# Optimization experiments

Hardware: AMD Instinct MI355X
Metric: run time of the kernel (lower is better)

## Reference

```python
import jax, jax.numpy as jnp
import numpy as np

N_NODES = 50000
N_EDGES = 800000
N_GRAPHS = 64
IN_DIM = 128
HID = 128
S, C = 4, 16
DIM1 = 3 * S * S  # 48
OUT_DIM = DIM1 * C  # 768


def gcn_conv(x, W, b, src, dst, w):
    """PyG GCNConv: linear transform, then sym-normalized aggregation with self-loops (weight 1)."""
    n = x.shape[0]
    h = x @ W  # [N, out]
    deg = jnp.zeros((n,), x.dtype).at[dst].add(w) + 1.0  # self-loop weight 1
    dinv = jax.lax.rsqrt(deg)
    norm = dinv[src] * w * dinv[dst]  # [E]
    agg = jnp.zeros_like(h).at[dst].add(h[src] * norm[:, None])
    agg = agg + h * (1.0 / deg)[:, None]  # self-loop messages
    return agg + b


def setup_inputs() -> dict:
    key = jax.random.key(0)
    ks = jax.random.split(key, 16)
    x = jax.random.normal(ks[0], (N_NODES, IN_DIM), jnp.float32)
    edge_index = jax.random.randint(ks[1], (2, N_EDGES), 0, N_NODES, jnp.int64)
    edge_attr = jax.random.uniform(ks[2], (N_EDGES,), jnp.float32)
    batch = jnp.sort(jax.random.randint(ks[3], (N_NODES,), 0, N_GRAPHS, jnp.int64))

    def glorot(k, fan_in, fan_out):
        s = np.sqrt(6.0 / (fan_in + fan_out)).astype(np.float32)
        return jax.random.uniform(k, (fan_in, fan_out), jnp.float32, -s, s)

    return {
        "x": x, "edge_index": edge_index, "edge_attr": edge_attr, "batch": batch,
        "W1": glorot(ks[4], IN_DIM, HID), "b1": jnp.zeros((HID,), jnp.float32),
        "W2": glorot(ks[5], HID, HID // 2), "b2": jnp.zeros((HID // 2,), jnp.float32),
        "W3": glorot(ks[6], HID // 2, HID // 4), "b3": jnp.zeros((HID // 4,), jnp.float32),
        "Wl": glorot(ks[7], HID // 4, OUT_DIM), "bl": jnp.zeros((OUT_DIM,), jnp.float32),
    }


def reference(x, edge_index, edge_attr, batch, W1, b1, W2, b2, W3, b3, Wl, bl):
    src, dst = edge_index[0], edge_index[1]
    w = edge_attr / edge_attr.max()
    h = jax.nn.relu(gcn_conv(x, W1, b1, src, dst, w))
    h = jax.nn.relu(gcn_conv(h, W2, b2, src, dst, w))
    h = jax.nn.relu(gcn_conv(h, W3, b3, src, dst, w))
    # global mean pool over graphs
    sums = jax.ops.segment_sum(h, batch, num_segments=N_GRAPHS)
    cnt = jax.ops.segment_sum(jnp.ones((h.shape[0],), h.dtype), batch, num_segments=N_GRAPHS)
    pooled = sums / jnp.maximum(cnt, 1.0)[:, None]
    out = pooled @ Wl + bl  # [G, OUT_DIM]
    return out.reshape(N_GRAPHS, DIM1, C)
```

## Files before the change

### kernel.cpp

```cpp
#include <hip/hip_runtime.h>
#include <hip/hip_bf16.h>

#define NN 50000
#define NE 800000
#define NG 64
#define OUTD 768

#define G1B ((NN + 63) / 64)
#define MAXB 128
#define SSEG 64
#define TTL 2
#define ESEG (NE / SSEG)
#define NTL (NN / TTL)
#define HRB (SSEG * TTL)

__device__ __forceinline__ float bflo(unsigned int u) { return __uint_as_float(u << 16); }
__device__ __forceinline__ float bfhi(unsigned int u) { return __uint_as_float(u & 0xffff0000u); }
__device__ __forceinline__ unsigned short f2bf(float f) {
    unsigned int u = __float_as_uint(f);
    return (unsigned short)((u + 0x7fffu + ((u >> 16) & 1u)) >> 16);
}
__device__ __forceinline__ unsigned int pack2bf(float lo, float hi) {
    return (unsigned int)f2bf(lo) | ((unsigned int)f2bf(hi) << 16);
}

typedef __attribute__((ext_vector_type(8))) short bf16x8;
typedef __attribute__((ext_vector_type(4))) float f32x4;
union FragU { uint4 u4; bf16x8 v; };

template <int K, int N>
constexpr int mfma_lds_bytes() { return (K / 32) * (N / 16) * 1024; }

template <int K, int N, typename TX>
__device__ __forceinline__ void mfma_gemm_body(char* smem,
                                               const TX* __restrict__ X,
                                               const float* __restrict__ W,
                                               unsigned short* __restrict__ Y,
                                               int nRows, int bx) {
    constexpr int NCT = N / 16;
    constexpr int KS = K / 32;
    const int tid = threadIdx.x;

    for (int q = tid; q < KS * NCT * 64; q += 256) {
        int lane = q & 63;
        int fi = q >> 6;
        int ct = fi % NCT, kc = fi / NCT;
        int col = ct * 16 + (lane & 15);
        int kb = kc * 32 + ((lane >> 4) << 3);
        uint4 w;
        w.x = pack2bf(W[(size_t)(kb + 0) * N + col], W[(size_t)(kb + 1) * N + col]);
        w.y = pack2bf(W[(size_t)(kb + 2) * N + col], W[(size_t)(kb + 3) * N + col]);
        w.z = pack2bf(W[(size_t)(kb + 4) * N + col], W[(size_t)(kb + 5) * N + col]);
        w.w = pack2bf(W[(size_t)(kb + 6) * N + col], W[(size_t)(kb + 7) * N + col]);
        *(uint4*)(smem + (size_t)q * 16) = w;
    }
    __syncthreads();

    const int lane = tid & 63;
    const int wv = tid >> 6;
    const int m = lane & 15;
    const int quad = lane >> 4;
    const int row = bx * 64 + wv * 16 + m;
    const bool rowok = row < nRows;
    const TX* xr = X + (size_t)(rowok ? row : 0) * K;

    f32x4 acc[NCT];
#pragma unroll
    for (int ct = 0; ct < NCT; ++ct) acc[ct] = (f32x4){0.f, 0.f, 0.f, 0.f};

#pragma unroll
    for (int kc = 0; kc < KS; ++kc) {
        const int k0 = kc * 32 + quad * 8;
        FragU a;
        if constexpr (sizeof(TX) == 4) {
            float4 a0 = make_float4(0.f, 0.f, 0.f, 0.f), a1 = a0;
            if (rowok) {
                a0 = *(const float4*)(xr + k0);
                a1 = *(const float4*)(xr + k0 + 4);
            }
            a.u4 = make_uint4(pack2bf(a0.x, a0.y), pack2bf(a0.z, a0.w),
                              pack2bf(a1.x, a1.y), pack2bf(a1.z, a1.w));
        } else {
            a.u4 = rowok ? *(const uint4*)(xr + k0) : make_uint4(0, 0, 0, 0);
        }
#pragma unroll
        for (int ct = 0; ct < NCT; ++ct) {
            FragU b;
            b.u4 = *(const uint4*)(smem + ((size_t)(kc * NCT + ct) * 64 + lane) * 16);
            acc[ct] = __builtin_amdgcn_mfma_f32_16x16x32_bf16(a.v, b.v, acc[ct], 0, 0, 0);
        }
    }

    const int orowb = bx * 64 + wv * 16 + quad * 4;
#pragma unroll
    for (int ct = 0; ct < NCT; ++ct) {
        int col = ct * 16 + m;
#pragma unroll
        for (int r = 0; r < 4; ++r) {
            int orow = orowb + r;
            if (orow < nRows) Y[(size_t)orow * N + col] = f2bf(acc[ct][r]);
        }
    }
}

template <int K, int N, typename TX>
__global__ __launch_bounds__(256) void mfma_gemm_kernel(const TX* __restrict__ X,
                                                        const float* __restrict__ W,
                                                        unsigned short* __restrict__ Y,
                                                        int nRows) {
    extern __shared__ char smem[];
    mfma_gemm_body<K, N>(smem, X, W, Y, nRows, blockIdx.x);
}

__global__ __launch_bounds__(256) void fused1_kernel(const float* __restrict__ x,
                                                     const float* __restrict__ W1,
                                                     unsigned short* __restrict__ bufA,
                                                     const float* __restrict__ ea,
                                                     unsigned int* wmax,
                                                     const int* __restrict__ dst,
                                                     int* __restrict__ rank,
                                                     unsigned short* __restrict__ pcnt) {
    extern __shared__ char smem[];
    const int b = blockIdx.x;
    if (b < G1B) {
        mfma_gemm_body<128, 128>(smem, x, W1, bufA, NN, b);
    } else if (b < G1B + MAXB) {
        float* red = (float*)smem;
        const int bb = b - G1B;
        const float4* ea4 = (const float4*)ea;
        float m = 0.0f;
        for (int i = bb * 256 + threadIdx.x; i < NE / 4; i += MAXB * 256) {
            float4 v = ea4[i];
            m = fmaxf(fmaxf(m, fmaxf(v.x, v.y)), fmaxf(v.z, v.w));
        }
        red[threadIdx.x] = m;
        __syncthreads();
        for (int off = 128; off > 0; off >>= 1) {
            if (threadIdx.x < off)
                red[threadIdx.x] = fmaxf(red[threadIdx.x], red[threadIdx.x + off]);
            __syncthreads();
        }
        if (threadIdx.x == 0) atomicMax(wmax, __float_as_uint(red[0]));
    } else {
        const int b2 = b - G1B - MAXB;
        const int seg = b2 >> 1;
        const int tile = b2 & 1;
        unsigned int* lcnt = (unsigned int*)smem;
        for (int i = threadIdx.x; i < NTL / 4; i += 256) lcnt[i] = 0;
        __syncthreads();
        const int base = seg * ESEG;
        const int nlo = tile * NTL;
        const int4* dst4 = (const int4*)(dst + base);
        for (int g = threadIdx.x; g < ESEG / 4; g += 256) {
            const int4 v = dst4[g];
            const int e0 = base + g * 4;
            const int dd[4] = {v.x, v.y, v.z, v.w};
#pragma unroll
            for (int j = 0; j < 4; ++j) {
                int d = dd[j] - nlo;
                if ((unsigned)d < (unsigned)NTL) {
                    unsigned sh = (unsigned)(d & 3) << 3;
                    unsigned old = atomicAdd(&lcnt[d >> 2], 1u << sh);
                    rank[e0 + j] = (int)((old >> sh) & 0xffu);
                }
            }
        }
        __syncthreads();
        unsigned short* prow = pcnt + (size_t)seg * NN + nlo;
        for (int i = threadIdx.x; i < NTL / 4; i += 256) {
            unsigned int w = lcnt[i];
            uint2 o;
            o.x = (w & 0xffu) | ((w & 0xff00u) << 8);
            o.y = ((w >> 16) & 0xffu) | ((w >> 8) & 0xff0000u);
            *(uint2*)(prow + i * 4) = o;
        }
    }
}

__global__ __launch_bounds__(256) void combscan_kernel(unsigned short* __restrict__ pcnt,
                                                       int* __restrict__ blocksum,
                                                       int* __restrict__ rowptr,
                                                       unsigned int* __restrict__ syncf) {
    __shared__ int sc[256];
    __shared__ int sb[256];
    const int tid = threadIdx.x;
    const int n = blockIdx.x * 256 + tid;
    int run = 0;
    if (n < NN) {
#pragma unroll 16
        for (int s = 0; s < SSEG; ++s) {
            size_t idx = (size_t)s * NN + n;
            int v = pcnt[idx];
            pcnt[idx] = (unsigned short)run;
            run += v;
        }
    }
    sc[tid] = run;
    __syncthreads();
    for (int off = 1; off < 256; off <<= 1) {
        int t = (tid >= off) ? sc[tid - off] : 0;
        __syncthreads();
        sc[tid] += t;
        __syncthreads();
    }
    if (tid == 0) blocksum[blockIdx.x] = sc[255];
    __threadfence();
    __syncthreads();
    if (tid == 0) {
        atomicAdd(syncf, 1u);
        while (atomicAdd(syncf, 0u) < (unsigned)gridDim.x) {}
    }
    __syncthreads();
    __threadfence();
    int bv = (tid < (int)gridDim.x) ? blocksum[tid] : 0;
    sb[tid] = bv;
    __syncthreads();
    for (int off = 1; off < 256; off <<= 1) {
        int t = (tid >= off) ? sb[tid - off] : 0;
        __syncthreads();
        sb[tid] += t;
        __syncthreads();
    }
    const int boff = (blockIdx.x > 0) ? sb[blockIdx.x - 1] : 0;
    if (n < NN) rowptr[n] = boff + sc[tid] - run;
    if (blockIdx.x == gridDim.x - 1 && tid == 0) rowptr[NN] = sb[gridDim.x - 1];
}

__global__ void scat_kernel(const int* __restrict__ src, const int* __restrict__ dst,
                            const float* __restrict__ ea,
                            const int* __restrict__ rowptr,
                            const unsigned short* __restrict__ pcnt,
                            const int* __restrict__ rank,
                            int2* __restrict__ epack, int nE) {
    int e = blockIdx.x * blockDim.x + threadIdx.x;
    if (e >= nE) return;
    int s = e / ESEG;
    int d = dst[e];
    int pos = rowptr[d] + (int)pcnt[(size_t)s * NN + d] + rank[e];
    epack[pos] = make_int2(src[e], __float_as_int(ea[e]));
}

__global__ void deg_kernel(const int2* __restrict__ epack, const int* __restrict__ rowptr,
                           const unsigned int* __restrict__ wmax,
                           float* __restrict__ nrm, float* __restrict__ invdeg, int n) {
    int i = blockIdx.x * blockDim.x + threadIdx.x;
    if (i >= n) return;
    float rw = 1.0f / __uint_as_float(*wmax);
    float srw = sqrtf(rw);
    int s0 = rowptr[i], s1 = rowptr[i + 1];
    float sa = 0.f, sb = 0.f;
    int e = s0;
    for (; e + 2 <= s1; e += 2) {
        sa += __int_as_float(epack[e].y);
        sb += __int_as_float(epack[e + 1].y);
    }
    if (e < s1) sa += __int_as_float(epack[e].y);
    float d = fmaf(sa + sb, rw, 1.0f);
    nrm[i] = rsqrtf(d) * srw;
    invdeg[i] = 1.0f / d;
}

template <int D>
__global__ __launch_bounds__(256) void agg_kernel(const unsigned short* __restrict__ H,
                                                  const int* __restrict__ rowptr,
                                                  const int2* __restrict__ epack,
                                                  const float* __restrict__ invdeg,
                                                  const float* __restrict__ nrm,
                                                  const float* __restrict__ bias,
                                                  unsigned short* __restrict__ out,
                                                  int nNodes) {
    constexpr int LPE = D / 8;
    constexpr int EPW = 64 / LPE;
    const int lane = threadIdx.x & 63;
    const int n = (blockIdx.x << 2) | (threadIdx.x >> 6);
    if (n >= nNodes) return;
    const int esub = lane / LPE;
    const int f8 = (lane % LPE) * 8;
    const int s0 = rowptr[n];
    const int cnt = rowptr[n + 1] - s0;
    const int2* ep = epack + s0;
    const float dn = nrm[n];

    float a[8] = {};
#define AGG8(c_, u_)                                                            \
    a[0] = fmaf(c_, bflo(u_.x), a[0]); a[1] = fmaf(c_, bfhi(u_.x), a[1]);       \
    a[2] = fmaf(c_, bflo(u_.y), a[2]); a[3] = fmaf(c_, bfhi(u_.y), a[3]);       \
    a[4] = fmaf(c_, bflo(u_.z), a[4]); a[5] = fmaf(c_, bfhi(u_.z), a[5]);       \
    a[6] = fmaf(c_, bflo(u_.w), a[6]); a[7] = fmaf(c_, bfhi(u_.w), a[7]);

    int kb = 0;
    for (; kb + 4 * EPW <= cnt; kb += 4 * EPW) {
        const int2 p0 = ep[kb + 0 * EPW + esub];
        const int2 p1 = ep[kb + 1 * EPW + esub];
        const int2 p2 = ep[kb + 2 * EPW + esub];
        const int2 p3 = ep[kb + 3 * EPW + esub];
        const uint4 u0 = *(const uint4*)(H + (size_t)p0.x * D + f8);
        const uint4 u1 = *(const uint4*)(H + (size_t)p1.x * D + f8);
        const uint4 u2 = *(const uint4*)(H + (size_t)p2.x * D + f8);
        const uint4 u3 = *(const uint4*)(H + (size_t)p3.x * D + f8);
        const float c0 = nrm[p0.x] * __int_as_float(p0.y) * dn;
        const float c1 = nrm[p1.x] * __int_as_float(p1.y) * dn;
        const float c2 = nrm[p2.x] * __int_as_float(p2.y) * dn;
        const float c3 = nrm[p3.x] * __int_as_float(p3.y) * dn;
        AGG8(c0, u0) AGG8(c1, u1) AGG8(c2, u2) AGG8(c3, u3)
    }
    for (; kb + 2 * EPW <= cnt; kb += 2 * EPW) {
        const int2 p0 = ep[kb + esub];
        const int2 p1 = ep[kb + EPW + esub];
        const uint4 u0 = *(const uint4*)(H + (size_t)p0.x * D + f8);
        const uint4 u1 = *(const uint4*)(H + (size_t)p1.x * D + f8);
        const float c0 = nrm[p0.x] * __int_as_float(p0.y) * dn;
        const float c1 = nrm[p1.x] * __int_as_float(p1.y) * dn;
        AGG8(c0, u0) AGG8(c1, u1)
    }
    for (; kb < cnt; kb += EPW) {
        const int idx = kb + esub;
        const bool ok = idx < cnt;
        const int2 p = ok ? ep[idx] : make_int2(n, 0);
        const uint4 u = *(const uint4*)(H + (size_t)p.x * D + f8);
        const float c = ok ? nrm[p.x] * __int_as_float(p.y) * dn : 0.f;
        AGG8(c, u)
    }
#undef AGG8
#pragma unroll
    for (int off = LPE; off < 64; off <<= 1) {
#pragma unroll
        for (int j = 0; j < 8; ++j) a[j] += __shfl_xor(a[j], off);
    }
    if (esub == 0) {
        const float id = invdeg[n];
        const uint4 un = *(const uint4*)(H + (size_t)n * D + f8);
        const float4 b0 = *(const float4*)(bias + f8);
        const float4 b1 = *(const float4*)(bias + f8 + 4);
        float o[8];
        o[0] = fmaxf(fmaf(id, bflo(un.x), a[0]) + b0.x, 0.f);
        o[1] = fmaxf(fmaf(id, bfhi(un.x), a[1]) + b0.y, 0.f);
        o[2] = fmaxf(fmaf(id, bflo(un.y), a[2]) + b0.z, 0.f);
        o[3] = fmaxf(fmaf(id, bfhi(un.y), a[3]) + b0.w, 0.f);
        o[4] = fmaxf(fmaf(id, bflo(un.z), a[4]) + b1.x, 0.f);
        o[5] = fmaxf(fmaf(id, bfhi(un.z), a[5]) + b1.y, 0.f);
        o[6] = fmaxf(fmaf(id, bflo(un.w), a[6]) + b1.z, 0.f);
        o[7] = fmaxf(fmaf(id, bfhi(un.w), a[7]) + b1.w, 0.f);
        uint4 w;
        w.x = pack2bf(o[0], o[1]);
        w.y = pack2bf(o[2], o[3]);
        w.z = pack2bf(o[4], o[5]);
        w.w = pack2bf(o[6], o[7]);
        *(uint4*)(out + (size_t)n * D + f8) = w;
    }
}

__global__ __launch_bounds__(1024) void poolfin_kernel(const unsigned short* __restrict__ h,
                                                       const int* __restrict__ batch,
                                                       const float* __restrict__ Wl,
                                                       const float* __restrict__ bl,
                                                       float* __restrict__ out, int n) {
    const int g = blockIdx.x;
    int lo = 0, hi = n;
    while (lo < hi) { int m = (lo + hi) >> 1; if (batch[m] < g) lo = m + 1; else hi = m; }
    const int start = lo;
    lo = start; hi = n;
    while (lo < hi) { int m = (lo + hi) >> 1; if (batch[m] < g + 1) lo = m + 1; else hi = m; }
    const int end = lo;

    __shared__ float part[1024];
    __shared__ float spool[32];
    const int f = threadIdx.x & 31;
    const int r = threadIdx.x >> 5;
    float acc = 0.f;
    for (int i = start + r; i < end; i += 32)
        acc += __uint_as_float((unsigned int)h[(size_t)i * 32 + f] << 16);
    part[threadIdx.x] = acc;
    __syncthreads();
    if (threadIdx.x < 32) {
        float s = 0.f;
#pragma unroll
        for (int q = 0; q < 32; ++q) s += part[q * 32 + f];
        float inv = 1.0f / fmaxf((float)(end - start), 1.0f);
        spool[f] = s * inv;
    }
    __syncthreads();
    if (threadIdx.x < OUTD) {
        const int o = threadIdx.x;
        float a2 = bl[o];
#pragma unroll
        for (int k = 0; k < 32; ++k)
            a2 = fmaf(spool[k], Wl[k * OUTD + o], a2);
        out[(size_t)g * OUTD + o] = a2;
    }
}

extern "C" void kernel_launch(void* const* d_in, const int* in_sizes, int n_in,
                              void* d_out, int out_size, void* d_ws, size_t ws_size,
                              hipStream_t stream) {
    const float* x = (const float*)d_in[0];
    const int* eidx = (const int*)d_in[1];
    const float* ea = (const float*)d_in[2];
    const int* batch = (const int*)d_in[3];
    const float* W1 = (const float*)d_in[4];
    const float* b1 = (const float*)d_in[5];
    const float* W2 = (const float*)d_in[6];
    const float* b2 = (const float*)d_in[7];
    const float* W3 = (const float*)d_in[8];
    const float* b3 = (const float*)d_in[9];
    const float* Wl = (const float*)d_in[10];
    const float* bl = (const float*)d_in[11];
    const int* src = eidx;
    const int* dst = eidx + NE;

    char* p = (char*)d_ws;
    auto take = [&](size_t bytes) {
        char* r = p;
        p += (bytes + 255) & ~(size_t)255;
        return r;
    };
    float* nrm = (float*)take(NN * 4);
    float* invdeg = (float*)take(NN * 4);
    int* rowptr = (int*)take((NN + 1) * 4);
    int* blocksum = (int*)take(256 * 4);
    int2* epack = (int2*)take((size_t)NE * 8);
    unsigned int* wmax = (unsigned int*)take(8);
    unsigned int* syncf = wmax + 1;
    unsigned short* bufA = (unsigned short*)take((size_t)NN * 128 * 2);
    unsigned short* bufB = (unsigned short*)take((size_t)NN * 128 * 2);
    int* rank = (int*)bufB;
    unsigned short* pcnt = (unsigned short*)((char*)bufB + (size_t)NE * 4 + 256);

    const int nblk = (NN + 255) / 256;
    const int eblk = (NE + 255) / 256;

    hipMemsetAsync(wmax, 0, 8, stream);

    constexpr int LDS1 = mfma_lds_bytes<128, 128>();
    static_assert(LDS1 >= NTL, "HR branch LDS (packed u8 counters) must fit");
    fused1_kernel<<<G1B + MAXB + HRB, 256, LDS1, stream>>>(x, W1, bufA, ea, wmax,
                                                           dst, rank, pcnt);
    combscan_kernel<<<nblk, 256, 0, stream>>>(pcnt, blocksum, rowptr, syncf);
    scat_kernel<<<eblk, 256, 0, stream>>>(src, dst, ea, rowptr, pcnt, rank, epack, NE);
    deg_kernel<<<nblk, 256, 0, stream>>>(epack, rowptr, wmax, nrm, invdeg, NN);

    agg_kernel<128><<<(NN + 3) / 4, 256, 0, stream>>>(bufA, rowptr, epack, invdeg, nrm, b1, bufB, NN);
    mfma_gemm_kernel<128, 64, unsigned short>
        <<<G1B, 256, mfma_lds_bytes<128, 64>(), stream>>>(bufB, W2, bufA, NN);
    agg_kernel<64><<<(NN + 3) / 4, 256, 0, stream>>>(bufA, rowptr, epack, invdeg, nrm, b2, bufB, NN);
    mfma_gemm_kernel<64, 32, unsigned short>
        <<<G1B, 256, mfma_lds_bytes<64, 32>(), stream>>>(bufB, W3, bufA, NN);
    agg_kernel<32><<<(NN + 3) / 4, 256, 0, stream>>>(bufA, rowptr, epack, invdeg, nrm, b3, bufB, NN);

    poolfin_kernel<<<NG, 1024, 0, stream>>>(bufB, batch, Wl, bl, (float*)d_out, NN);
}
```

Measured before the change: 277.0 us.

## Cache per-edge normalized coefficients in first aggregation and reuse in later layers

The first aggregation layer now writes the fully normalized edge coefficient (nrm[src]*w*nrm[dst]) back into the edge pack, and the next two layers read it directly instead of gathering nrm[src] per edge. The number of histogram segments is halved with the scan loop fully unrolled. The grid barrier in the combined scan uses atomics plus s_sleep. This removes a random gather per edge in two layers, at the cost of extra stores in layer one and fewer, wider partial counters.

```diff
diff --git a/kernel.cpp b/kernel.cpp
--- a/kernel.cpp
+++ b/kernel.cpp
@@ -8,7 +8,7 @@
 
 #define G1B ((NN + 63) / 64)
 #define MAXB 128
-#define SSEG 64
+#define SSEG 32
 #define TTL 2
 #define ESEG (NE / SSEG)
 #define NTL (NN / TTL)
@@ -187,7 +187,7 @@
     const int n = blockIdx.x * 256 + tid;
     int run = 0;
     if (n < NN) {
-#pragma unroll 16
+#pragma unroll
         for (int s = 0; s < SSEG; ++s) {
             size_t idx = (size_t)s * NN + n;
             int v = pcnt[idx];
@@ -203,16 +203,15 @@
         sc[tid] += t;
         __syncthreads();
     }
-    if (tid == 0) blocksum[blockIdx.x] = sc[255];
-    __threadfence();
-    __syncthreads();
     if (tid == 0) {
+        atomicExch(&blocksum[blockIdx.x], sc[255]);
+        __threadfence();
         atomicAdd(syncf, 1u);
-        while (atomicAdd(syncf, 0u) < (unsigned)gridDim.x) {}
-    }
-    __syncthreads();
-    __threadfence();
-    int bv = (tid < (int)gridDim.x) ? blocksum[tid] : 0;
+        while (atomicAdd(syncf, 0u) < (unsigned)gridDim.x)
+            __builtin_amdgcn_s_sleep(2);
+    }
+    __syncthreads();
+    int bv = (tid < (int)gridDim.x) ? atomicAdd(&blocksum[tid], 0) : 0;
     sb[tid] = bv;
     __syncthreads();
     for (int off = 1; off < 256; off <<= 1) {
@@ -260,10 +259,10 @@
     invdeg[i] = 1.0f / d;
 }
 
-template <int D>
+template <int D, bool PRE>
 __global__ __launch_bounds__(256) void agg_kernel(const unsigned short* __restrict__ H,
                                                   const int* __restrict__ rowptr,
-                                                  const int2* __restrict__ epack,
+                                                  int2* __restrict__ epack,
                                                   const float* __restrict__ invdeg,
                                                   const float* __restrict__ nrm,
                                                   const float* __restrict__ bias,
@@ -278,8 +277,8 @@
     const int f8 = (lane % LPE) * 8;
     const int s0 = rowptr[n];
     const int cnt = rowptr[n + 1] - s0;
-    const int2* ep = epack + s0;
-    const float dn = nrm[n];
+    int2* ep = epack + s0;
+    const float dn = PRE ? 1.0f : nrm[n];
 
     float a[8] = {};
 #define AGG8(c_, u_)                                                            \
@@ -298,10 +297,22 @@
         const uint4 u1 = *(const uint4*)(H + (size_t)p1.x * D + f8);
         const uint4 u2 = *(const uint4*)(H + (size_t)p2.x * D + f8);
         const uint4 u3 = *(const uint4*)(H + (size_t)p3.x * D + f8);
-        const float c0 = nrm[p0.x] * __int_as_float(p0.y) * dn;
-        const float c1 = nrm[p1.x] * __int_as_float(p1.y) * dn;
-        const float c2 = nrm[p2.x] * __int_as_float(p2.y) * dn;
-        const float c3 = nrm[p3.x] * __int_as_float(p3.y) * dn;
+        float c0, c1, c2, c3;
+        if constexpr (PRE) {
+            c0 = __int_as_float(p0.y); c1 = __int_as_float(p1.y);
+            c2 = __int_as_float(p2.y); c3 = __int_as_float(p3.y);
+        } else {
+            c0 = nrm[p0.x] * __int_as_float(p0.y) * dn;
+            c1 = nrm[p1.x] * __int_as_float(p1.y) * dn;
+            c2 = nrm[p2.x] * __int_as_float(p2.y) * dn;
+            c3 = nrm[p3.x] * __int_as_float(p3.y) * dn;
+            if (f8 == 0) {
+                ep[kb + 0 * EPW + esub].y = __float_as_int(c0);
+                ep[kb + 1 * EPW + esub].y = __float_as_int(c1);
+                ep[kb + 2 * EPW + esub].y = __float_as_int(c2);
+                ep[kb + 3 * EPW + esub].y = __float_as_int(c3);
+            }
+        }
         AGG8(c0, u0) AGG8(c1, u1) AGG8(c2, u2) AGG8(c3, u3)
     }
     for (; kb + 2 * EPW <= cnt; kb += 2 * EPW) {
@@ -309,8 +320,17 @@
         const int2 p1 = ep[kb + EPW + esub];
         const uint4 u0 = *(const uint4*)(H + (size_t)p0.x * D + f8);
         const uint4 u1 = *(const uint4*)(H + (size_t)p1.x * D + f8);
-        const float c0 = nrm[p0.x] * __int_as_float(p0.y) * dn;
-        const float c1 = nrm[p1.x] * __int_as_float(p1.y) * dn;
+        float c0, c1;
+        if constexpr (PRE) {
+            c0 = __int_as_float(p0.y); c1 = __int_as_float(p1.y);
+        } else {
+            c0 = nrm[p0.x] * __int_as_float(p0.y) * dn;
+            c1 = nrm[p1.x] * __int_as_float(p1.y) * dn;
+            if (f8 == 0) {
+                ep[kb + esub].y = __float_as_int(c0);
+                ep[kb + EPW + esub].y = __float_as_int(c1);
+            }
+        }
         AGG8(c0, u0) AGG8(c1, u1)
     }
     for (; kb < cnt; kb += EPW) {
@@ -318,7 +338,13 @@
         const bool ok = idx < cnt;
         const int2 p = ok ? ep[idx] : make_int2(n, 0);
         const uint4 u = *(const uint4*)(H + (size_t)p.x * D + f8);
-        const float c = ok ? nrm[p.x] * __int_as_float(p.y) * dn : 0.f;
+        float c;
+        if constexpr (PRE) {
+            c = ok ? __int_as_float(p.y) : 0.f;
+        } else {
+            c = ok ? nrm[p.x] * __int_as_float(p.y) * dn : 0.f;
+            if (ok && f8 == 0) ep[idx].y = __float_as_int(c);
+        }
         AGG8(c, u)
     }
 #undef AGG8
@@ -439,13 +465,13 @@
     scat_kernel<<<eblk, 256, 0, stream>>>(src, dst, ea, rowptr, pcnt, rank, epack, NE);
     deg_kernel<<<nblk, 256, 0, stream>>>(epack, rowptr, wmax, nrm, invdeg, NN);
 
-    agg_kernel<128><<<(NN + 3) / 4, 256, 0, stream>>>(bufA, rowptr, epack, invdeg, nrm, b1, bufB, NN);
+    agg_kernel<128, false><<<(NN + 3) / 4, 256, 0, stream>>>(bufA, rowptr, epack, invdeg, nrm, b1, bufB, NN);
     mfma_gemm_kernel<128, 64, unsigned short>
         <<<G1B, 256, mfma_lds_bytes<128, 64>(), stream>>>(bufB, W2, bufA, NN);
-    agg_kernel<64><<<(NN + 3) / 4, 256, 0, stream>>>(bufA, rowptr, epack, invdeg, nrm, b2, bufB, NN);
+    agg_kernel<64, true><<<(NN + 3) / 4, 256, 0, stream>>>(bufA, rowptr, epack, invdeg, nrm, b2, bufB, NN);
     mfma_gemm_kernel<64, 32, unsigned short>
         <<<G1B, 256, mfma_lds_bytes<64, 32>(), stream>>>(bufB, W3, bufA, NN);
-    agg_kernel<32><<<(NN + 3) / 4, 256, 0, stream>>>(bufA, rowptr, epack, invdeg, nrm, b3, bufB, NN);
+    agg_kernel<32, true><<<(NN + 3) / 4, 256, 0, stream>>>(bufA, rowptr, epack, invdeg, nrm, b3, bufB, NN);
 
     poolfin_kernel<<<NG, 1024, 0, stream>>>(bufB, batch, Wl, bl, (float*)d_out, NN);
 }
```

Result: faster. 257.9 us (-6.9%).
